# Performance work log

Hardware: AMD Instinct MI355X
Metric: run time of the kernel (lower is better)

Reference implementation:

```python
import jax, jax.numpy as jnp
import numpy as np

B, P, D = 8, 1024, 1024
H, N = 16, 64  # num_heads, head_dim


def setup_inputs() -> dict:
    key = jax.random.key(0)
    k1, k2, k3 = jax.random.split(key, 3)
    inputs = jax.random.normal(k1, (B, P, D), dtype=jnp.float32)
    # Keras 'random_normal' initializer: stddev 0.05
    w_qkv = jax.random.normal(k2, (H, 3, D, N), dtype=jnp.float32) * 0.05
    w_o = jax.random.normal(k3, (N * H, D), dtype=jnp.float32) * 0.05
    return {"inputs": inputs, "w_qkv": w_qkv, "w_o": w_o}


def reference(inputs, w_qkv, w_o):
    # Per-head QKV projection: [b,p,d] x [h,3,d,n] -> [b,h,3,p,n]
    proj = jnp.einsum('bpv,havn->bhapn', inputs, w_qkv)
    q = proj[:, :, 0]  # [b,h,p,n]
    k = proj[:, :, 1]
    v = proj[:, :, 2]
    head_dim = q.shape[-1]
    scale = 1.0 / jnp.sqrt(jnp.asarray(head_dim, dtype=jnp.float32))
    scores = jnp.einsum('bhqn,bhkn->bhqk', q, k) * scale  # [b,h,p,p]
    attn = jax.nn.softmax(scores, axis=-1)
    out = jnp.einsum('bhqk,bhkn->bhqn', attn, v)  # [b,h,p,n]
    # concat heads along feature dim: [b,p,h*n]
    b, h, p, n = out.shape
    concat = out.transpose(0, 2, 1, 3).reshape(b, p, h * n)
    return jnp.einsum('bpi,ij->bpj', concat, w_o)  # [b,p,d_model]
```

## Files before the change

### kernel.cpp

```cpp
#include <hip/hip_runtime.h>
#include <stdint.h>

typedef _Float16 f16;
typedef __attribute__((ext_vector_type(2))) _Float16 f16x2;
typedef __attribute__((ext_vector_type(4))) _Float16 f16x4;
typedef __attribute__((ext_vector_type(8))) _Float16 f16x8;
typedef __attribute__((ext_vector_type(2))) __fp16 h16x2;
typedef __attribute__((ext_vector_type(4))) float f32x4;
typedef __attribute__((ext_vector_type(4))) uint32_t u32x4;

__device__ __forceinline__ void gload_lds16(const void* g, void* l) {
  __builtin_amdgcn_global_load_lds(
      (__attribute__((address_space(1))) void*)const_cast<void*>(g),
      (__attribute__((address_space(3))) void*)l, 16, 0, 0);
}


__global__ void convert_x(const float* __restrict__ in, f16* __restrict__ out) {
  int i = blockIdx.x * 256 + threadIdx.x;
  float4 v = ((const float4*)in)[i];
  f16x4 hv;
  hv[0] = (f16)v.x; hv[1] = (f16)v.y; hv[2] = (f16)v.z; hv[3] = (f16)v.w;
  ((f16x4*)out)[i] = hv;
}

__global__ void transpose_wqkv(const float* __restrict__ in, f16* __restrict__ out) {
  __shared__ float tile[64][65];
  int s = blockIdx.x >> 4;
  int vt = blockIdx.x & 15;
  int hh = s / 3, a = s - hh * 3;
  int tx = threadIdx.x & 63, ty = threadIdx.x >> 6;
#pragma unroll
  for (int i = 0; i < 16; i++) {
    int r = i * 4 + ty;
    tile[r][tx] = in[((size_t)(s * 1024 + vt * 64 + r)) * 64 + tx];
  }
  __syncthreads();
#pragma unroll
  for (int i = 0; i < 16; i++) {
    int n = i * 4 + ty;
    out[((size_t)(a * 1024 + hh * 64 + n)) * 1024 + vt * 64 + tx] = (f16)tile[tx][n];
  }
}

__global__ void transpose_wo(const float* __restrict__ in, f16* __restrict__ out) {
  __shared__ float tile[64][65];
  int rt = blockIdx.x >> 4, ct = blockIdx.x & 15;
  int tx = threadIdx.x & 63, ty = threadIdx.x >> 6;
#pragma unroll
  for (int i = 0; i < 16; i++) {
    int r = i * 4 + ty;
    tile[r][tx] = in[((size_t)(rt * 64 + r)) * 1024 + ct * 64 + tx];
  }
  __syncthreads();
#pragma unroll
  for (int i = 0; i < 16; i++) {
    int j = i * 4 + ty;
    out[((size_t)(ct * 64 + j)) * 1024 + rt * 64 + tx] = (f16)tile[tx][j];
  }
}

template <int OUTMODE>
__global__ __launch_bounds__(256, 2) void gemm_kernel(
    const f16* __restrict__ A, const f16* __restrict__ BT, void* __restrict__ out,
    void* __restrict__ out2, int M, int N, int K) {
  __shared__ __align__(16) f16 As[128][64];
  __shared__ __align__(16) f16 Bs[128][64];
  const int t = threadIdx.x;
  const int lane = t & 63, wave = t >> 6;
  const int lr = lane & 15, lg = lane >> 4;
  const int wm = wave >> 1, wn = wave & 1;
  const int nTN = N >> 7;
  const int bm = blockIdx.x / nTN, bn = blockIdx.x % nTN;
  const f16* Ab = A + (size_t)bm * 128 * K;
  const f16* Bb = BT + (size_t)bn * 128 * K;

  const f32x4 zero4 = {0.f, 0.f, 0.f, 0.f};
  f32x4 acc[4][4];
#pragma unroll
  for (int m = 0; m < 4; m++)
#pragma unroll
    for (int n = 0; n < 4; n++) acc[m][n] = zero4;

  for (int k0 = 0; k0 < K; k0 += 64) {
    __syncthreads();
#pragma unroll
    for (int i = 0; i < 4; i++) {
      int q = wave * 4 + i;
      int u = q * 64 + lane;
      int r = u >> 3, j = u & 7;
      gload_lds16(Ab + (size_t)r * K + k0 + ((j ^ (r & 7)) << 3),
                  (char*)&As[0][0] + q * 1024);
      gload_lds16(Bb + (size_t)r * K + k0 + ((j ^ (r & 7)) << 3),
                  (char*)&Bs[0][0] + q * 1024);
    }
    __syncthreads();
#pragma unroll
    for (int half = 0; half < 2; half++) {
      f16x8 af[4], bf[4];
#pragma unroll
      for (int m = 0; m < 4; m++) {
        int r = wm * 64 + m * 16 + lr;
        af[m] = *(const f16x8*)&As[r][((half * 4 + lg) ^ (r & 7)) << 3];
      }
#pragma unroll
      for (int n = 0; n < 4; n++) {
        int r = wn * 64 + n * 16 + lr;
        bf[n] = *(const f16x8*)&Bs[r][((half * 4 + lg) ^ (r & 7)) << 3];
      }
#pragma unroll
      for (int m = 0; m < 4; m++)
#pragma unroll
        for (int n = 0; n < 4; n++)
          acc[m][n] = __builtin_amdgcn_mfma_f32_16x16x32_f16(af[m], bf[n], acc[m][n], 0, 0, 0);
    }
  }

  const int r0 = bm * 128 + wm * 64;
  const int c0 = bn * 128 + wn * 64;
  if (OUTMODE == 2 && bn >= 16) {
    f16* VT = (f16*)out2;
    const int bb = bm >> 3;
#pragma unroll
    for (int m = 0; m < 4; m++) {
      int pl = (r0 + m * 16 + lg * 4) & 1023;
      int pl2 = (pl & 992) | ((pl & 12) << 1) | ((pl & 16) >> 2);
#pragma unroll
      for (int n = 0; n < 4; n++) {
        int vcol = c0 - 2048 + n * 16 + lr;
        f16x4 pv;
#pragma unroll
        for (int i = 0; i < 4; i++) pv[i] = (f16)acc[m][n][i];
        *(f16x4*)&VT[((size_t)(bb * 16 + (vcol >> 6)) * 64 + (vcol & 63)) * 1024 + pl2] = pv;
      }
    }
  } else {
#pragma unroll
    for (int m = 0; m < 4; m++)
#pragma unroll
      for (int n = 0; n < 4; n++)
#pragma unroll
        for (int i = 0; i < 4; i++) {
          int gr = r0 + m * 16 + lg * 4 + i;
          int gc = c0 + n * 16 + lr;
          if (OUTMODE == 1)
            ((float*)out)[(size_t)gr * N + gc] = acc[m][n][i];
          else
            ((f16*)out)[(size_t)gr * N + gc] = (f16)acc[m][n][i];
        }
  }
}

__global__ __launch_bounds__(256, 4) void attn_kernel(
    const f16* __restrict__ QKV, const f16* __restrict__ VT, f16* __restrict__ C) {
  __shared__ __align__(16) f16 smem[16384];

  const int t = threadIdx.x, lane = t & 63, wave = t >> 6;
  const int lr = lane & 15, lg = lane >> 4;
  const int bh = blockIdx.x, pt = blockIdx.y;
  const int b = bh >> 4, h = bh & 15;
  const int p0 = pt * 128;

  const f16* Qg = QKV + ((size_t)(b * 1024 + p0)) * 3072 + h * 64;
  const f16* Kg = QKV + ((size_t)(b * 1024)) * 3072 + 1024 + h * 64;
  const f16* Vg = VT + (size_t)bh * 64 * 1024;

#pragma unroll
  for (int i = 0; i < 4; i++) {
    int q = wave * 4 + i;
    int u = q * 64 + lane;
    int r = u >> 3, j = u & 7;
    gload_lds16(Qg + (size_t)r * 3072 + ((j ^ (r & 7)) << 3), (char*)smem + q * 1024);
  }
  __syncthreads();

  const f16 qscale = (f16)0.180336878f;
  f16x8 qa[2][2];
#pragma unroll
  for (int m = 0; m < 2; m++)
#pragma unroll
    for (int hh = 0; hh < 2; hh++) {
      int r = wave * 32 + m * 16 + lr;
      f16x8 v = *(const f16x8*)&smem[(size_t)r * 64 + (((hh * 4 + lg) ^ (lr & 7)) << 3)];
#pragma unroll
      for (int e = 0; e < 8; e++) v[e] *= qscale;
      qa[m][hh] = v;
    }
  __syncthreads();

  auto STAGE = [&](int kc, int cur) {
#pragma unroll
    for (int i = 0; i < 2; i++) {
      int q = wave * 2 + i;
      int u = q * 64 + lane;
      int r = u >> 3, j = u & 7;
      gload_lds16(Kg + (size_t)(kc * 64 + r) * 3072 + ((j ^ (r & 7)) << 3),
                  (char*)smem + cur * 16384 + q * 1024);
      gload_lds16(Vg + (size_t)r * 1024 + kc * 64 + ((j ^ (r & 7)) << 3),
                  (char*)smem + cur * 16384 + 8192 + q * 1024);
    }
  };

  STAGE(0, 0);
  STAGE(1, 1);
  __syncthreads();

  const f32x4 zero4 = {0.f, 0.f, 0.f, 0.f};
  f32x4 o[2][4], o_l[2];
#pragma unroll
  for (int m = 0; m < 2; m++) {
    o_l[m] = zero4;
#pragma unroll
    for (int n = 0; n < 4; n++) o[m][n] = zero4;
  }
  const f32x4 sInit = {-8.f, -8.f, -8.f, -8.f};
  const f16x8 ones8 = {(f16)1.f, (f16)1.f, (f16)1.f, (f16)1.f,
                       (f16)1.f, (f16)1.f, (f16)1.f, (f16)1.f};

#pragma unroll 1
  for (int kc = 0; kc < 16; kc++) {
    const int cur = kc & 1;
    const int kB = cur * 8192;
    const char* vB = (const char*)smem + cur * 16384 + 8192;

    f32x4 s[2][4];
#pragma unroll
    for (int m = 0; m < 2; m++)
#pragma unroll
      for (int kb = 0; kb < 4; kb++) s[m][kb] = sInit;
    __builtin_amdgcn_s_setprio(1);
#pragma unroll
    for (int kb = 0; kb < 4; kb++) {
      int r = kb * 16 + lr;
      f16x8 kf0 = *(const f16x8*)&smem[kB + (size_t)r * 64 + ((lg ^ (lr & 7)) << 3)];
      f16x8 kf1 = *(const f16x8*)&smem[kB + (size_t)r * 64 + (((4 + lg) ^ (lr & 7)) << 3)];
#pragma unroll
      for (int m = 0; m < 2; m++) {
        s[m][kb] = __builtin_amdgcn_mfma_f32_16x16x32_f16(kf0, qa[m][0], s[m][kb], 0, 0, 0);
        s[m][kb] = __builtin_amdgcn_mfma_f32_16x16x32_f16(kf1, qa[m][1], s[m][kb], 0, 0, 0);
      }
    }
    __builtin_amdgcn_s_setprio(0);

    f16x8 pa8[2][2];
#pragma unroll
    for (int m = 0; m < 2; m++)
#pragma unroll
      for (int j = 0; j < 2; j++) {
        uint32_t w0, w1, w2, w3;
        w0 = __builtin_bit_cast(uint32_t, __builtin_amdgcn_cvt_pkrtz(exp2f(s[m][2 * j][0]), exp2f(s[m][2 * j][1])));
        w1 = __builtin_bit_cast(uint32_t, __builtin_amdgcn_cvt_pkrtz(exp2f(s[m][2 * j][2]), exp2f(s[m][2 * j][3])));
        w2 = __builtin_bit_cast(uint32_t, __builtin_amdgcn_cvt_pkrtz(exp2f(s[m][2 * j + 1][0]), exp2f(s[m][2 * j + 1][1])));
        w3 = __builtin_bit_cast(uint32_t, __builtin_amdgcn_cvt_pkrtz(exp2f(s[m][2 * j + 1][2]), exp2f(s[m][2 * j + 1][3])));
        u32x4 ww = {w0, w1, w2, w3};
        pa8[m][j] = __builtin_bit_cast(f16x8, ww);
      }

    __builtin_amdgcn_s_setprio(1);
#pragma unroll
    for (int j = 0; j < 2; j++) {
      o_l[0] = __builtin_amdgcn_mfma_f32_16x16x32_f16(pa8[0][j], ones8, o_l[0], 0, 0, 0);
      o_l[1] = __builtin_amdgcn_mfma_f32_16x16x32_f16(pa8[1][j], ones8, o_l[1], 0, 0, 0);
#pragma unroll
      for (int n = 0; n < 4; n++) {
        int rv = n * 16 + lr;
        f16x8 vb = *(const f16x8*)(vB + (size_t)rv * 128 + (((4 * j + lg) ^ (lr & 7)) << 4));
        o[0][n] = __builtin_amdgcn_mfma_f32_16x16x32_f16(pa8[0][j], vb, o[0][n], 0, 0, 0);
        o[1][n] = __builtin_amdgcn_mfma_f32_16x16x32_f16(pa8[1][j], vb, o[1][n], 0, 0, 0);
      }
    }
    __builtin_amdgcn_s_setprio(0);

    __syncthreads();
    if (kc + 2 < 16) STAGE(kc + 2, cur);
  }

#pragma unroll
  for (int m = 0; m < 2; m++)
#pragma unroll
    for (int i = 0; i < 4; i++) {
      float li = 1.f / o_l[m][i];
      int prow = p0 + wave * 32 + m * 16 + lg * 4 + i;
#pragma unroll
      for (int n = 0; n < 4; n++) {
        int col = h * 64 + n * 16 + lr;
        C[((size_t)(b * 1024 + prow)) * 1024 + col] = (f16)(o[m][n][i] * li);
      }
    }
}

extern "C" void kernel_launch(void* const* d_in, const int* in_sizes, int n_in,
                              void* d_out, int out_size, void* d_ws, size_t ws_size,
                              hipStream_t stream) {
  const float* X = (const float*)d_in[0];
  const float* Wqkv = (const float*)d_in[1];
  const float* Wo = (const float*)d_in[2];
  float* Y = (float*)d_out;

  f16* ws = (f16*)d_ws;
  f16* X16 = ws;
  f16* WqkvT = ws + 8388608;
  f16* WoT = ws + 11534336;
  f16* QKV = ws + 12582912;
  f16* VT = (f16*)d_out;

  convert_x<<<8192, 256, 0, stream>>>(X, X16);
  transpose_wqkv<<<768, 256, 0, stream>>>(Wqkv, WqkvT);
  transpose_wo<<<256, 256, 0, stream>>>(Wo, WoT);
  gemm_kernel<2><<<64 * 24, 256, 0, stream>>>(X16, WqkvT, QKV, VT, 8192, 3072, 1024);
  attn_kernel<<<dim3(128, 8), 256, 0, stream>>>(QKV, VT, X16 );
  gemm_kernel<1><<<64 * 8, 256, 0, stream>>>(X16 , WoT, Y, nullptr, 8192, 1024, 1024);
}
```

Before: 159.6 us.

## Add dedicated 256x192-tile pipelined QKV projection GEMM with XCD-aware block remap

```diff
diff --git a/kernel.cpp b/kernel.cpp
--- a/kernel.cpp
+++ b/kernel.cpp
@@ -5,7 +5,6 @@
 typedef __attribute__((ext_vector_type(2))) _Float16 f16x2;
 typedef __attribute__((ext_vector_type(4))) _Float16 f16x4;
 typedef __attribute__((ext_vector_type(8))) _Float16 f16x8;
-typedef __attribute__((ext_vector_type(2))) __fp16 h16x2;
 typedef __attribute__((ext_vector_type(4))) float f32x4;
 typedef __attribute__((ext_vector_type(4))) uint32_t u32x4;
 
@@ -60,10 +59,162 @@
   }
 }
 
-template <int OUTMODE>
-__global__ __launch_bounds__(256, 2) void gemm_kernel(
-    const f16* __restrict__ A, const f16* __restrict__ BT, void* __restrict__ out,
-    void* __restrict__ out2, int M, int N, int K) {
+__global__ __launch_bounds__(512, 2) void gemm_qkv_kernel(
+    const f16* __restrict__ A, const f16* __restrict__ BT, f16* __restrict__ out,
+    f16* __restrict__ VT) {
+  constexpr int K = 1024;
+  __shared__ __align__(16) f16 smem[57344];
+  const int t = threadIdx.x;
+  const int lane = t & 63, wave = t >> 6;
+  const int lr = lane & 15, lg = lane >> 4;
+  const int wm = wave >> 2, wn = wave & 3;
+  const int bid = blockIdx.x;
+  const int wg = (bid & 7) * 64 + (bid >> 3);
+  const int bm = wg >> 4, bn = wg & 15;
+  const f16* Ab = A + (size_t)bm * 256 * K;
+  const f16* Bb = BT + (size_t)bn * 192 * K;
+
+  auto STAGE_A = [&](int kt, int buf) {
+    const f16* src = Ab + kt * 64;
+    char* dst = (char*)smem + buf * 32768;
+#pragma unroll
+    for (int i = 0; i < 4; i++) {
+      int g = i * 512 + t;
+      int r = g >> 3, p = g & 7;
+      gload_lds16(src + (size_t)r * K + ((p ^ (r & 7)) << 3),
+                  dst + (i * 512 + wave * 64) * 16);
+    }
+  };
+  auto STAGE_B = [&](int kt, int buf) {
+    const f16* src = Bb + kt * 64;
+    char* dst = (char*)smem + 65536 + buf * 24576;
+#pragma unroll
+    for (int i = 0; i < 3; i++) {
+      int g = i * 512 + t;
+      int r = g >> 3, p = g & 7;
+      gload_lds16(src + (size_t)r * K + ((p ^ (r & 7)) << 3),
+                  dst + (i * 512 + wave * 64) * 16);
+    }
+  };
+
+  const f32x4 zero4 = {0.f, 0.f, 0.f, 0.f};
+  f32x4 acc[8][3];
+#pragma unroll
+  for (int m = 0; m < 8; m++)
+#pragma unroll
+    for (int n = 0; n < 3; n++) acc[m][n] = zero4;
+
+  STAGE_A(0, 0);
+  STAGE_B(0, 0);
+  asm volatile("s_waitcnt vmcnt(0)" ::: "memory");
+  __builtin_amdgcn_s_barrier();
+
+#pragma unroll 2
+  for (int kt = 0; kt < 16; kt++) {
+    const int cur = kt & 1;
+    const f16* AL = smem + cur * 16384;
+    const f16* BL = smem + 32768 + cur * 12288;
+    const bool pf = (kt + 1) < 16;
+
+    f16x8 bf[3], af[4];
+#pragma unroll
+    for (int n = 0; n < 3; n++) {
+      int rb = wn * 48 + n * 16 + lr;
+      bf[n] = *(const f16x8*)&BL[rb * 64 + ((lg ^ (rb & 7)) << 3)];
+    }
+#pragma unroll
+    for (int m = 0; m < 4; m++) {
+      int r = wm * 128 + m * 16 + lr;
+      af[m] = *(const f16x8*)&AL[r * 64 + ((lg ^ (r & 7)) << 3)];
+    }
+    if (pf) STAGE_A(kt + 1, cur ^ 1);
+    __builtin_amdgcn_s_setprio(1);
+#pragma unroll
+    for (int m = 0; m < 4; m++)
+#pragma unroll
+      for (int n = 0; n < 3; n++)
+        acc[m][n] = __builtin_amdgcn_mfma_f32_16x16x32_f16(af[m], bf[n], acc[m][n], 0, 0, 0);
+    __builtin_amdgcn_s_setprio(0);
+
+#pragma unroll
+    for (int m = 0; m < 4; m++) {
+      int r = wm * 128 + (4 + m) * 16 + lr;
+      af[m] = *(const f16x8*)&AL[r * 64 + ((lg ^ (r & 7)) << 3)];
+    }
+    if (pf) STAGE_B(kt + 1, cur ^ 1);
+    __builtin_amdgcn_s_setprio(1);
+#pragma unroll
+    for (int m = 0; m < 4; m++)
+#pragma unroll
+      for (int n = 0; n < 3; n++)
+        acc[4 + m][n] = __builtin_amdgcn_mfma_f32_16x16x32_f16(af[m], bf[n], acc[4 + m][n], 0, 0, 0);
+    __builtin_amdgcn_s_setprio(0);
+
+#pragma unroll
+    for (int n = 0; n < 3; n++) {
+      int rb = wn * 48 + n * 16 + lr;
+      bf[n] = *(const f16x8*)&BL[rb * 64 + (((4 + lg) ^ (rb & 7)) << 3)];
+    }
+#pragma unroll
+    for (int m = 0; m < 4; m++) {
+      int r = wm * 128 + m * 16 + lr;
+      af[m] = *(const f16x8*)&AL[r * 64 + (((4 + lg) ^ (r & 7)) << 3)];
+    }
+    __builtin_amdgcn_s_setprio(1);
+#pragma unroll
+    for (int m = 0; m < 4; m++)
+#pragma unroll
+      for (int n = 0; n < 3; n++)
+        acc[m][n] = __builtin_amdgcn_mfma_f32_16x16x32_f16(af[m], bf[n], acc[m][n], 0, 0, 0);
+    __builtin_amdgcn_s_setprio(0);
+
+#pragma unroll
+    for (int m = 0; m < 4; m++) {
+      int r = wm * 128 + (4 + m) * 16 + lr;
+      af[m] = *(const f16x8*)&AL[r * 64 + (((4 + lg) ^ (r & 7)) << 3)];
+    }
+    __builtin_amdgcn_s_setprio(1);
+#pragma unroll
+    for (int m = 0; m < 4; m++)
+#pragma unroll
+      for (int n = 0; n < 3; n++)
+        acc[4 + m][n] = __builtin_amdgcn_mfma_f32_16x16x32_f16(af[m], bf[n], acc[4 + m][n], 0, 0, 0);
+    __builtin_amdgcn_s_setprio(0);
+
+    asm volatile("s_waitcnt vmcnt(0)" ::: "memory");
+    __builtin_amdgcn_s_barrier();
+  }
+
+  const int r0 = bm * 256 + wm * 128;
+  const int c0 = bn * 192 + wn * 48;
+  const int bb = bm >> 2;
+#pragma unroll
+  for (int m = 0; m < 8; m++) {
+    int pl = (r0 + m * 16 + lg * 4) & 1023;
+    int pl2 = (pl & 992) | ((pl & 12) << 1) | ((pl & 16) >> 2);
+#pragma unroll
+    for (int n = 0; n < 3; n++) {
+      int gcb = c0 + n * 16;
+      if (gcb >= 2048) {
+        int vcol = gcb - 2048 + lr;
+        f16x4 pv;
+#pragma unroll
+        for (int i = 0; i < 4; i++) pv[i] = (f16)acc[m][n][i];
+        *(f16x4*)&VT[((size_t)(bb * 16 + (vcol >> 6)) * 64 + (vcol & 63)) * 1024 + pl2] = pv;
+      } else {
+#pragma unroll
+        for (int i = 0; i < 4; i++) {
+          int gr = r0 + m * 16 + lg * 4 + i;
+          out[(size_t)gr * 3072 + gcb + lr] = (f16)acc[m][n][i];
+        }
+      }
+    }
+  }
+}
+
+__global__ __launch_bounds__(256, 2) void gemm_out_kernel(
+    const f16* __restrict__ A, const f16* __restrict__ BT, float* __restrict__ out,
+    int M, int N, int K) {
   __shared__ __align__(16) f16 As[128][64];
   __shared__ __align__(16) f16 Bs[128][64];
   const int t = threadIdx.x;
@@ -118,37 +269,16 @@
 
   const int r0 = bm * 128 + wm * 64;
   const int c0 = bn * 128 + wn * 64;
-  if (OUTMODE == 2 && bn >= 16) {
-    f16* VT = (f16*)out2;
-    const int bb = bm >> 3;
-#pragma unroll
-    for (int m = 0; m < 4; m++) {
-      int pl = (r0 + m * 16 + lg * 4) & 1023;
-      int pl2 = (pl & 992) | ((pl & 12) << 1) | ((pl & 16) >> 2);
-#pragma unroll
-      for (int n = 0; n < 4; n++) {
-        int vcol = c0 - 2048 + n * 16 + lr;
-        f16x4 pv;
-#pragma unroll
-        for (int i = 0; i < 4; i++) pv[i] = (f16)acc[m][n][i];
-        *(f16x4*)&VT[((size_t)(bb * 16 + (vcol >> 6)) * 64 + (vcol & 63)) * 1024 + pl2] = pv;
-      }
-    }
-  } else {
-#pragma unroll
-    for (int m = 0; m < 4; m++)
-#pragma unroll
-      for (int n = 0; n < 4; n++)
-#pragma unroll
-        for (int i = 0; i < 4; i++) {
-          int gr = r0 + m * 16 + lg * 4 + i;
-          int gc = c0 + n * 16 + lr;
-          if (OUTMODE == 1)
-            ((float*)out)[(size_t)gr * N + gc] = acc[m][n][i];
-          else
-            ((f16*)out)[(size_t)gr * N + gc] = (f16)acc[m][n][i];
-        }
-  }
+#pragma unroll
+  for (int m = 0; m < 4; m++)
+#pragma unroll
+    for (int n = 0; n < 4; n++)
+#pragma unroll
+      for (int i = 0; i < 4; i++) {
+        int gr = r0 + m * 16 + lg * 4 + i;
+        int gc = c0 + n * 16 + lr;
+        out[(size_t)gr * N + gc] = acc[m][n][i];
+      }
 }
 
 __global__ __launch_bounds__(256, 4) void attn_kernel(
@@ -307,7 +437,7 @@
   convert_x<<<8192, 256, 0, stream>>>(X, X16);
   transpose_wqkv<<<768, 256, 0, stream>>>(Wqkv, WqkvT);
   transpose_wo<<<256, 256, 0, stream>>>(Wo, WoT);
-  gemm_kernel<2><<<64 * 24, 256, 0, stream>>>(X16, WqkvT, QKV, VT, 8192, 3072, 1024);
+  gemm_qkv_kernel<<<512, 512, 0, stream>>>(X16, WqkvT, QKV, VT);
   attn_kernel<<<dim3(128, 8), 256, 0, stream>>>(QKV, VT, X16 );
-  gemm_kernel<1><<<64 * 8, 256, 0, stream>>>(X16 , WoT, Y, nullptr, 8192, 1024, 1024);
-}
+  gemm_out_kernel<<<64 * 8, 256, 0, stream>>>(X16 , WoT, Y, 8192, 1024, 1024);
+}
```

Result: no change. 160.7 us (+0.6%).

## Rewrite QKV GEMM with 256x128 tiles, triple-buffered async LDS loads

Applied to the files above, without the earlier changes.

```diff
diff --git a/kernel.cpp b/kernel.cpp
--- a/kernel.cpp
+++ b/kernel.cpp
@@ -5,7 +5,6 @@
 typedef __attribute__((ext_vector_type(2))) _Float16 f16x2;
 typedef __attribute__((ext_vector_type(4))) _Float16 f16x4;
 typedef __attribute__((ext_vector_type(8))) _Float16 f16x8;
-typedef __attribute__((ext_vector_type(2))) __fp16 h16x2;
 typedef __attribute__((ext_vector_type(4))) float f32x4;
 typedef __attribute__((ext_vector_type(4))) uint32_t u32x4;
 
@@ -60,10 +59,124 @@
   }
 }
 
-template <int OUTMODE>
-__global__ __launch_bounds__(256, 2) void gemm_kernel(
-    const f16* __restrict__ A, const f16* __restrict__ BT, void* __restrict__ out,
-    void* __restrict__ out2, int M, int N, int K) {
+__global__ __launch_bounds__(512, 2) void gemm_qkv_kernel(
+    const f16* __restrict__ A, const f16* __restrict__ BT, f16* __restrict__ out,
+    f16* __restrict__ VT) {
+  constexpr int K = 1024;
+  __shared__ __align__(16) f16 smem[73728];
+  const int t = threadIdx.x;
+  const int lane = t & 63, wave = t >> 6;
+  const int lr = lane & 15, lg = lane >> 4;
+  const int wm = wave >> 1, wn = wave & 1;
+  const int bid = blockIdx.x;
+  const int wg = (bid & 7) * 96 + (bid >> 3);
+  const int bm = wg / 24, bn = wg % 24;
+  const f16* Ab = A + (size_t)bm * 256 * K;
+  const f16* Bb = BT + (size_t)bn * 128 * K;
+
+  auto STAGE = [&](int kt, int buf) {
+    const f16* srcA = Ab + kt * 64;
+    char* dstA = (char*)(smem + buf * 16384);
+#pragma unroll
+    for (int i = 0; i < 4; i++) {
+      int g = i * 512 + t;
+      int r = g >> 3, p = g & 7;
+      gload_lds16(srcA + (size_t)r * K + ((p ^ (r & 7)) << 3),
+                  dstA + (i * 512 + wave * 64) * 16);
+    }
+    const f16* srcB = Bb + kt * 64;
+    char* dstB = (char*)(smem + 49152 + buf * 8192);
+#pragma unroll
+    for (int i = 0; i < 2; i++) {
+      int g = i * 512 + t;
+      int r = g >> 3, p = g & 7;
+      gload_lds16(srcB + (size_t)r * K + ((p ^ (r & 7)) << 3),
+                  dstB + (i * 512 + wave * 64) * 16);
+    }
+  };
+
+  const f32x4 zero4 = {0.f, 0.f, 0.f, 0.f};
+  f32x4 acc[4][4];
+#pragma unroll
+  for (int m = 0; m < 4; m++)
+#pragma unroll
+    for (int n = 0; n < 4; n++) acc[m][n] = zero4;
+
+  STAGE(0, 0);
+  STAGE(1, 1);
+  asm volatile("s_waitcnt vmcnt(6)" ::: "memory");
+  __builtin_amdgcn_s_barrier();
+
+  int cur = 0, nxt2 = 2;
+#pragma unroll 1
+  for (int kt = 0; kt < 16; kt++) {
+    const f16* AL = smem + cur * 16384;
+    const f16* BL = smem + 49152 + cur * 8192;
+
+    if (kt + 2 < 16) STAGE(kt + 2, nxt2);
+
+#pragma unroll
+    for (int ks = 0; ks < 2; ks++) {
+      f16x8 af[4], bf[4];
+#pragma unroll
+      for (int m = 0; m < 4; m++) {
+        int r = wm * 64 + m * 16 + lr;
+        af[m] = *(const f16x8*)&AL[r * 64 + (((ks * 4 + lg) ^ (r & 7)) << 3)];
+      }
+#pragma unroll
+      for (int n = 0; n < 4; n++) {
+        int rb = wn * 64 + n * 16 + lr;
+        bf[n] = *(const f16x8*)&BL[rb * 64 + (((ks * 4 + lg) ^ (rb & 7)) << 3)];
+      }
+      __builtin_amdgcn_s_setprio(1);
+#pragma unroll
+      for (int m = 0; m < 4; m++)
+#pragma unroll
+        for (int n = 0; n < 4; n++)
+          acc[m][n] = __builtin_amdgcn_mfma_f32_16x16x32_f16(af[m], bf[n], acc[m][n], 0, 0, 0);
+      __builtin_amdgcn_s_setprio(0);
+    }
+
+    if (kt < 14) {
+      asm volatile("s_waitcnt vmcnt(6)" ::: "memory");
+    } else {
+      asm volatile("s_waitcnt vmcnt(0)" ::: "memory");
+    }
+    __builtin_amdgcn_s_barrier();
+    cur = (cur == 2) ? 0 : cur + 1;
+    nxt2 = (nxt2 == 2) ? 0 : nxt2 + 1;
+  }
+
+  const int r0 = bm * 256 + wm * 64;
+  const int c0 = bn * 128 + wn * 64;
+  const int bb = bm >> 2;
+#pragma unroll
+  for (int m = 0; m < 4; m++) {
+    int pl = (r0 + m * 16 + lg * 4) & 1023;
+    int pl2 = (pl & 992) | ((pl & 12) << 1) | ((pl & 16) >> 2);
+#pragma unroll
+    for (int n = 0; n < 4; n++) {
+      int gcb = c0 + n * 16;
+      if (gcb >= 2048) {
+        int vcol = gcb - 2048 + lr;
+        f16x4 pv;
+#pragma unroll
+        for (int i = 0; i < 4; i++) pv[i] = (f16)acc[m][n][i];
+        *(f16x4*)&VT[((size_t)(bb * 16 + (vcol >> 6)) * 64 + (vcol & 63)) * 1024 + pl2] = pv;
+      } else {
+#pragma unroll
+        for (int i = 0; i < 4; i++) {
+          int gr = r0 + m * 16 + lg * 4 + i;
+          out[(size_t)gr * 3072 + gcb + lr] = (f16)acc[m][n][i];
+        }
+      }
+    }
+  }
+}
+
+__global__ __launch_bounds__(256, 2) void gemm_out_kernel(
+    const f16* __restrict__ A, const f16* __restrict__ BT, float* __restrict__ out,
+    int M, int N, int K) {
   __shared__ __align__(16) f16 As[128][64];
   __shared__ __align__(16) f16 Bs[128][64];
   const int t = threadIdx.x;
@@ -118,37 +231,16 @@
 
   const int r0 = bm * 128 + wm * 64;
   const int c0 = bn * 128 + wn * 64;
-  if (OUTMODE == 2 && bn >= 16) {
-    f16* VT = (f16*)out2;
-    const int bb = bm >> 3;
-#pragma unroll
-    for (int m = 0; m < 4; m++) {
-      int pl = (r0 + m * 16 + lg * 4) & 1023;
-      int pl2 = (pl & 992) | ((pl & 12) << 1) | ((pl & 16) >> 2);
-#pragma unroll
-      for (int n = 0; n < 4; n++) {
-        int vcol = c0 - 2048 + n * 16 + lr;
-        f16x4 pv;
-#pragma unroll
-        for (int i = 0; i < 4; i++) pv[i] = (f16)acc[m][n][i];
-        *(f16x4*)&VT[((size_t)(bb * 16 + (vcol >> 6)) * 64 + (vcol & 63)) * 1024 + pl2] = pv;
-      }
-    }
-  } else {
-#pragma unroll
-    for (int m = 0; m < 4; m++)
-#pragma unroll
-      for (int n = 0; n < 4; n++)
-#pragma unroll
-        for (int i = 0; i < 4; i++) {
-          int gr = r0 + m * 16 + lg * 4 + i;
-          int gc = c0 + n * 16 + lr;
-          if (OUTMODE == 1)
-            ((float*)out)[(size_t)gr * N + gc] = acc[m][n][i];
-          else
-            ((f16*)out)[(size_t)gr * N + gc] = (f16)acc[m][n][i];
-        }
-  }
+#pragma unroll
+  for (int m = 0; m < 4; m++)
+#pragma unroll
+    for (int n = 0; n < 4; n++)
+#pragma unroll
+      for (int i = 0; i < 4; i++) {
+        int gr = r0 + m * 16 + lg * 4 + i;
+        int gc = c0 + n * 16 + lr;
+        out[(size_t)gr * N + gc] = acc[m][n][i];
+      }
 }
 
 __global__ __launch_bounds__(256, 4) void attn_kernel(
@@ -307,7 +399,7 @@
   convert_x<<<8192, 256, 0, stream>>>(X, X16);
   transpose_wqkv<<<768, 256, 0, stream>>>(Wqkv, WqkvT);
   transpose_wo<<<256, 256, 0, stream>>>(Wo, WoT);
-  gemm_kernel<2><<<64 * 24, 256, 0, stream>>>(X16, WqkvT, QKV, VT, 8192, 3072, 1024);
+  gemm_qkv_kernel<<<768, 512, 0, stream>>>(X16, WqkvT, QKV, VT);
   attn_kernel<<<dim3(128, 8), 256, 0, stream>>>(QKV, VT, X16 );
-  gemm_kernel<1><<<64 * 8, 256, 0, stream>>>(X16 , WoT, Y, nullptr, 8192, 1024, 1024);
-}
+  gemm_out_kernel<<<64 * 8, 256, 0, stream>>>(X16 , WoT, Y, 8192, 1024, 1024);
+}
```

New measurement: 168.5 us. +5.6%, slower.
